# Kernel optimization log

Measured on AMD Instinct MI355X. Metric: run time of the kernel, lower is better.

## Reference

```python
import jax, jax.numpy as jnp
import numpy as np

HID = 512      # LSTM hidden per direction (1024 // 2)
EMB = 768      # BERT hidden size
NUM_TAG = 9
B, S = 64, 512


def setup_inputs() -> dict:
    key = jax.random.key(0)
    ks = jax.random.split(key, 12)
    g = lambda k, sh, sc: (jax.random.normal(k, sh, jnp.float32) * sc)
    return {
        "x": jax.random.normal(ks[0], (B, S, EMB), jnp.float32),
        "mask": jnp.ones((B, S), jnp.int32),
        "target_tag": jax.random.randint(ks[1], (B, S), 0, NUM_TAG, jnp.int32),
        "w_ih_f": g(ks[2], (4 * HID, EMB), 0.02),
        "w_hh_f": g(ks[3], (4 * HID, HID), 0.02),
        "b_f": jnp.zeros((4 * HID,), jnp.float32),
        "w_ih_b": g(ks[4], (4 * HID, EMB), 0.02),
        "w_hh_b": g(ks[5], (4 * HID, HID), 0.02),
        "b_b": jnp.zeros((4 * HID,), jnp.float32),
        "w_out": g(ks[6], (NUM_TAG, 2 * HID), 0.02),
        "b_out": jnp.zeros((NUM_TAG,), jnp.float32),
        "start_trans": g(ks[7], (NUM_TAG,), 0.1),
        "end_trans": g(ks[8], (NUM_TAG,), 0.1),
        "trans": g(ks[9], (NUM_TAG, NUM_TAG), 0.1),
    }


def _lstm_dir(x, w_ih, w_hh, b, reverse):
    # x: [B,S,E] -> outputs [S,B,H]; PyTorch gate order i,f,g,o
    xp = jnp.einsum('bse,ge->sbg', x, w_ih) + b  # precompute input proj [S,B,4H]
    if reverse:
        xp = xp[::-1]
    Bq = x.shape[0]
    def step(carry, xt):
        h, c = carry
        pre = xt + h @ w_hh.T
        i, f, g_, o = jnp.split(pre, 4, axis=-1)
        c = jax.nn.sigmoid(f) * c + jax.nn.sigmoid(i) * jnp.tanh(g_)
        h = jax.nn.sigmoid(o) * jnp.tanh(c)
        return (h, c), h
    init = (jnp.zeros((Bq, HID), x.dtype), jnp.zeros((Bq, HID), x.dtype))
    _, hs = jax.lax.scan(step, init, xp)
    if reverse:
        hs = hs[::-1]
    return hs


def _crf_nll_token_mean(emis, tags, m, start_trans, end_trans, trans):
    # emis: [S,B,T] time-major; tags: [S,B] int; m: [S,B] float (mask)
    Sq, Bq, T = emis.shape
    bidx = jnp.arange(Bq)
    # ---- numerator: score of the gold path ----
    num = start_trans[tags[0]] + emis[0, bidx, tags[0]]
    trans_steps = trans[tags[:-1], tags[1:]]                                   # [S-1,B]
    emit_steps = jnp.take_along_axis(emis[1:], tags[1:, :, None], axis=2)[..., 0]
    num = num + ((trans_steps + emit_steps) * m[1:]).sum(0)
    last_idx = m.sum(0).astype(jnp.int32) - 1                                   # [B]
    num = num + end_trans[tags[last_idx, bidx]]
    # ---- denominator: forward algorithm (log-sum-exp recursion) ----
    alpha0 = start_trans + emis[0]                                              # [B,T]
    def step(alpha, em):
        emis_t, m_t = em
        nxt = jax.nn.logsumexp(alpha[:, :, None] + trans[None] + emis_t[:, None, :], axis=1)
        return jnp.where(m_t[:, None] > 0, nxt, alpha), None
    alpha, _ = jax.lax.scan(step, alpha0, (emis[1:], m[1:]))
    den = jax.nn.logsumexp(alpha + end_trans, axis=1)
    llh = num - den
    return -(llh.sum() / m.sum())  # reduction='token_mean', negated (model loss)


def reference(x, mask, target_tag, w_ih_f, w_hh_f, b_f, w_ih_b, w_hh_b, b_b,
              w_out, b_out, start_trans, end_trans, trans):
    hf = _lstm_dir(x, w_ih_f, w_hh_f, b_f, reverse=False)   # [S,B,H]
    hb = _lstm_dir(x, w_ih_b, w_hh_b, b_b, reverse=True)    # [S,B,H]
    h = jnp.concatenate([hf, hb], axis=-1)                  # [S,B,2H]
    emis = jnp.einsum('sbh,th->sbt', h, w_out) + b_out      # [S,B,T] (dropout=identity in eval)
    tags = target_tag.T                                     # [S,B]
    m = mask.T.astype(emis.dtype)                           # [S,B]
    return _crf_nll_token_mean(emis, tags, m, start_trans, end_trans, trans)
```

## Files before the change

### kernel.cpp

```cpp
#include <hip/hip_runtime.h>
#include <cstdint>
#include <cstddef>

#define SS   512
#define BB   64
#define EMBD 768
#define HIDN 512
#define G4   2048
#define NTAG 9

typedef __attribute__((ext_vector_type(8))) __bf16 bf16x8;
typedef __attribute__((ext_vector_type(4))) float  f32x4;
typedef unsigned long long u64;

union HCast { f32x4 f; bf16x8 h; };

__device__ inline void load_h16_bypass(const void* base, f32x4* f) {
  asm volatile(
    "global_load_dwordx4 %0, %16, off sc0 sc1\n\t"
    "global_load_dwordx4 %1, %16, off offset:64 sc0 sc1\n\t"
    "global_load_dwordx4 %2, %16, off offset:128 sc0 sc1\n\t"
    "global_load_dwordx4 %3, %16, off offset:192 sc0 sc1\n\t"
    "global_load_dwordx4 %4, %16, off offset:256 sc0 sc1\n\t"
    "global_load_dwordx4 %5, %16, off offset:320 sc0 sc1\n\t"
    "global_load_dwordx4 %6, %16, off offset:384 sc0 sc1\n\t"
    "global_load_dwordx4 %7, %16, off offset:448 sc0 sc1\n\t"
    "global_load_dwordx4 %8, %16, off offset:512 sc0 sc1\n\t"
    "global_load_dwordx4 %9, %16, off offset:576 sc0 sc1\n\t"
    "global_load_dwordx4 %10, %16, off offset:640 sc0 sc1\n\t"
    "global_load_dwordx4 %11, %16, off offset:704 sc0 sc1\n\t"
    "global_load_dwordx4 %12, %16, off offset:768 sc0 sc1\n\t"
    "global_load_dwordx4 %13, %16, off offset:832 sc0 sc1\n\t"
    "global_load_dwordx4 %14, %16, off offset:896 sc0 sc1\n\t"
    "global_load_dwordx4 %15, %16, off offset:960 sc0 sc1\n\t"
    "s_waitcnt vmcnt(0)"
    : "=&v"(f[0]), "=&v"(f[1]), "=&v"(f[2]), "=&v"(f[3]),
      "=&v"(f[4]), "=&v"(f[5]), "=&v"(f[6]), "=&v"(f[7]),
      "=&v"(f[8]), "=&v"(f[9]), "=&v"(f[10]), "=&v"(f[11]),
      "=&v"(f[12]), "=&v"(f[13]), "=&v"(f[14]), "=&v"(f[15])
    : "v"(base)
    : "memory");
}
__device__ inline void store_h8_bypass(void* p, u64 v) {
  asm volatile("global_store_dwordx2 %0, %1, off sc0 sc1" :: "v"(p), "v"(v) : "memory");
}
__device__ inline void store_i32_bypass(int* p, int v) {
  asm volatile("global_store_dword %0, %1, off sc0 sc1" :: "v"(p), "v"(v) : "memory");
}
__device__ inline int load_i32_bypass(const int* p) {
  int v;
  asm volatile("global_load_dword %0, %1, off sc0 sc1\n\ts_waitcnt vmcnt(0)"
               : "=v"(v) : "v"(p) : "memory");
  return v;
}

__global__ __launch_bounds__(256) void cvt_kernel(
    const float* __restrict__ src, __bf16* __restrict__ dst, int n8)
{
  int i = blockIdx.x * 256 + threadIdx.x;
  if (i >= n8) return;
  f32x4 a = *reinterpret_cast<const f32x4*>(src + 8 * (size_t)i);
  f32x4 b = *reinterpret_cast<const f32x4*>(src + 8 * (size_t)i + 4);
  bf16x8 o;
  o[0]=(__bf16)a[0]; o[1]=(__bf16)a[1]; o[2]=(__bf16)a[2]; o[3]=(__bf16)a[3];
  o[4]=(__bf16)b[0]; o[5]=(__bf16)b[1]; o[6]=(__bf16)b[2]; o[7]=(__bf16)b[3];
  *reinterpret_cast<bf16x8*>(dst + 8 * (size_t)i) = o;
}

__global__ __launch_bounds__(256, 2) void proj_kernel(
    const __bf16* __restrict__ xb, const __bf16* __restrict__ wfb,
    const __bf16* __restrict__ wbb, const float* __restrict__ bias_f,
    const float* __restrict__ bias_b, float* __restrict__ xp,
    int t0, int chunk)
{
  const int nb = blockIdx.x;
  const int tt = blockIdx.y;
  const int d  = blockIdx.z;
  const int s  = d ? (SS - 1 - (t0 + tt)) : (t0 + tt);
  const __bf16* __restrict__ wih = d ? wbb : wfb;
  const float*  __restrict__ bias = d ? bias_b : bias_f;

  const int t = threadIdx.x, wv = t >> 6, l = t & 63;
  const int quad = l >> 4, col = l & 15;

  const __bf16* brow[8];
  float bj[8];
  const int pbase = 128 * nb;
#pragma unroll
  for (int j = 0; j < 8; j++) {
    int p    = pbase + 16 * j + col;
    int gate = p & 3;
    int hc   = 16 * (p >> 6) + 4 * ((p >> 2) & 3) + ((p >> 4) & 3);
    int g    = gate * HIDN + hc;
    brow[j]  = wih + (size_t)g * EMBD + 8 * quad;
    bj[j]    = bias[g];
  }
  const __bf16* arow = xb + ((size_t)(16 * wv + col) * SS + s) * EMBD + 8 * quad;

  f32x4 acc[8];
#pragma unroll
  for (int j = 0; j < 8; j++) acc[j] = f32x4{0.f, 0.f, 0.f, 0.f};

  for (int kk = 0; kk < 24; kk++) {
    bf16x8 a = *reinterpret_cast<const bf16x8*>(arow + 32 * kk);
#pragma unroll
    for (int j = 0; j < 8; j++) {
      bf16x8 b = *reinterpret_cast<const bf16x8*>(brow[j] + 32 * kk);
      acc[j] = __builtin_amdgcn_mfma_f32_16x16x32_bf16(a, b, acc[j], 0, 0, 0);
    }
  }
  float* xpd = xp + (size_t)(d * chunk + tt) * (size_t)G4 * BB + 16 * wv + 4 * quad;
#pragma unroll
  for (int j = 0; j < 8; j++) {
    int p = pbase + 16 * j + col;
    f32x4 v = acc[j];
    v[0] += bj[j]; v[1] += bj[j]; v[2] += bj[j]; v[3] += bj[j];
    *reinterpret_cast<f32x4*>(xpd + (size_t)p * BB) = v;
  }
}

struct RecCtl {
  int prog[2][64];
  int pad[128];
};

struct RecParams {
  const float* xp;
  const float* whh_f;
  const float* whh_b;
  __bf16* hh;
  float*  cT;
  RecCtl* ctl;
  int     chunk;
};

__global__ __launch_bounds__(256, 1) void rec_kernel(RecParams p)
{
  const int wg   = blockIdx.x;
  const int d    = wg >> 5;
  const int sl   = wg & 31;
  const int t    = threadIdx.x;
  const int wv   = t >> 6;
  const int l    = t & 63;
  const int quad = l >> 4;
  const int col  = l & 15;
  const int hcl  = col >> 2;
  const int gate = col & 3;
  const int j4   = col & 3;

  const float* __restrict__ whh = d ? p.whh_b : p.whh_f;

  bf16x8 bfrag[4][16];
#pragma unroll
  for (int j = 0; j < 4; j++) {
    const int hcb = 16 * sl + 4 * hcl + j;
    const float* wr = whh + (size_t)(gate * HIDN + hcb) * HIDN + 8 * quad;
#pragma unroll
    for (int kk = 0; kk < 16; kk++) {
      f32x4 w0 = *reinterpret_cast<const f32x4*>(wr + 32 * kk);
      f32x4 w1 = *reinterpret_cast<const f32x4*>(wr + 32 * kk + 4);
      bf16x8 v;
      v[0] = (__bf16)w0[0]; v[1] = (__bf16)w0[1]; v[2] = (__bf16)w0[2]; v[3] = (__bf16)w0[3];
      v[4] = (__bf16)w1[0]; v[5] = (__bf16)w1[1]; v[6] = (__bf16)w1[2]; v[7] = (__bf16)w1[3];
      bfrag[j][kk] = v;
    }
  }

  const int bA = 16 * wv + col;
  const int bC = 16 * wv + 4 * quad + gate;
  const int hcs = 16 * sl + 4 * hcl;
  const size_t slotsz = (size_t)BB * HIDN;
  __bf16* hhd = p.hh + (size_t)d * (p.chunk + 1) * slotsz;
  const float* xpd = p.xp + (size_t)d * p.chunk * ((size_t)G4 * BB);

  float c[4];
#pragma unroll
  for (int j = 0; j < 4; j++)
    c[j] = p.cT[((size_t)d * HIDN + hcs + j) * BB + bC];

  f32x4 xpn[4];
#pragma unroll
  for (int j = 0; j < 4; j++)
    xpn[j] = *reinterpret_cast<const f32x4*>(
        xpd + (size_t)(64 * sl + 16 * j + col) * BB + 16 * wv + 4 * quad);

  int* prog = &p.ctl->prog[d][0];
  const int* myslot = prog + (l & 31);

  u64 hword = 0;
  for (int tt = 0; tt < p.chunk; tt++) {
    const char* hbase = (const char*)hhd + (size_t)tt * slotsz * 2
                      + (size_t)bA * (HIDN * 2) + quad * 16;
    f32x4 araw[16];
    load_h16_bypass(hbase, araw);
    bf16x8 afrag[16];
#pragma unroll
    for (int kk = 0; kk < 16; kk++) { HCast hc_; hc_.f = araw[kk]; afrag[kk] = hc_.h; }

    f32x4 acc[4][2];
#pragma unroll
    for (int j = 0; j < 4; j++) {
      acc[j][0] = xpn[j];
      acc[j][1] = f32x4{0.f, 0.f, 0.f, 0.f};
    }
#pragma unroll
    for (int kk = 0; kk < 16; kk += 2) {
#pragma unroll
      for (int j = 0; j < 4; j++) {
        acc[j][0] = __builtin_amdgcn_mfma_f32_16x16x32_bf16(afrag[kk],     bfrag[j][kk],     acc[j][0], 0, 0, 0);
        acc[j][1] = __builtin_amdgcn_mfma_f32_16x16x32_bf16(afrag[kk + 1], bfrag[j][kk + 1], acc[j][1], 0, 0, 0);
      }
    }

    hword = 0;
#pragma unroll
    for (int j = 0; j < 4; j++) {
      float v0 = acc[j][0][0] + acc[j][1][0];
      float v1 = acc[j][0][1] + acc[j][1][1];
      float v2 = acc[j][0][2] + acc[j][1][2];
      float v3 = acc[j][0][3] + acc[j][1][3];
      {
        float t0 = __shfl_xor(v1, 1); float t1 = __shfl_xor(v0, 1);
        float t2 = __shfl_xor(v3, 1); float t3 = __shfl_xor(v2, 1);
        if (j4 & 1) { v0 = t0; v2 = t2; } else { v1 = t1; v3 = t3; }
        float u0 = __shfl_xor(v2, 2); float u1 = __shfl_xor(v3, 2);
        float u2 = __shfl_xor(v0, 2); float u3 = __shfl_xor(v1, 2);
        if (j4 & 2) { v0 = u0; v1 = u1; } else { v2 = u2; v3 = u3; }
      }
      float ig = 1.f / (1.f + __expf(-v0));
      float fg = 1.f / (1.f + __expf(-v1));
      float gg = 1.f - 2.f / (__expf(2.f * v2) + 1.f);
      float og = 1.f / (1.f + __expf(-v3));
      c[j] = fg * c[j] + ig * gg;
      float hn = og * (1.f - 2.f / (__expf(2.f * c[j]) + 1.f));
      union { __bf16 b; unsigned short u; } cv; cv.b = (__bf16)hn;
      hword |= (u64)cv.u << (16 * j);
    }
    store_h8_bypass((char*)hhd + (size_t)(tt + 1) * slotsz * 2
                    + (size_t)bC * (HIDN * 2) + (size_t)hcs * 2, hword);

    if (tt + 1 < p.chunk) {
#pragma unroll
      for (int j = 0; j < 4; j++)
        xpn[j] = *reinterpret_cast<const f32x4*>(
            xpd + (size_t)(tt + 1) * ((size_t)G4 * BB)
            + (size_t)(64 * sl + 16 * j + col) * BB + 16 * wv + 4 * quad);
    }

    __builtin_amdgcn_s_waitcnt(0);
    __syncthreads();
    if (t == 0) store_i32_bypass(prog + sl, tt + 1);
    if (wv == 0) {
      const int tgt = tt + 1;
      while (true) {
        int v = load_i32_bypass(myslot);
        if (__ballot(v >= tgt) == ~0ull) break;
        __builtin_amdgcn_s_sleep(1);
      }
    }
    __syncthreads();
    __atomic_signal_fence(__ATOMIC_SEQ_CST);
  }

  store_h8_bypass((char*)hhd + (size_t)bC * (HIDN * 2) + (size_t)hcs * 2, hword);
#pragma unroll
  for (int j = 0; j < 4; j++)
    p.cT[((size_t)d * HIDN + hcs + j) * BB + bC] = c[j];
}

__global__ __launch_bounds__(256) void emis_kernel(
    const __bf16* __restrict__ hh, const float* __restrict__ w_out,
    float* __restrict__ emis_f, float* __restrict__ emis_b,
    int t0, int chunk)
{
  const int tt = blockIdx.x;
  const int d  = blockIdx.y;
  const int t  = threadIdx.x;
  const int b  = t & 63;
  const int grp = t >> 6;

  const __bf16* hp = hh + ((size_t)d * (chunk + 1) + tt + 1) * ((size_t)BB * HIDN)
                   + (size_t)b * HIDN;
  const float* w0 = w_out + (size_t)grp * (2 * HIDN) + d * HIDN;
  const float* w1 = w_out + (size_t)(grp + 4) * (2 * HIDN) + d * HIDN;
  const float* w2 = w_out + (size_t)8 * (2 * HIDN) + d * HIDN;

  float a0 = 0.f, a1 = 0.f, a2 = 0.f;
  for (int k = 0; k < HIDN; k += 8) {
    bf16x8 hv8 = *reinterpret_cast<const bf16x8*>(hp + k);
#pragma unroll
    for (int j = 0; j < 8; j++) {
      float hv = (float)hv8[j];
      a0 += hv * w0[k + j];
      a1 += hv * w1[k + j];
      a2 += hv * w2[k + j];
    }
  }
  const int sidx = (d == 0) ? (t0 + tt) : (SS - 1 - (t0 + tt));
  float* dst = d ? emis_b : emis_f;
  dst[((size_t)sidx * BB + b) * NTAG + grp]     = a0;
  dst[((size_t)sidx * BB + b) * NTAG + grp + 4] = a1;
  if (grp == 0) dst[((size_t)sidx * BB + b) * NTAG + 8] = a2;
}

__global__ __launch_bounds__(64) void crf_kernel(
    const float* __restrict__ emis_f, const float* __restrict__ emis_b,
    const float* __restrict__ b_out, const float* __restrict__ start_tr,
    const float* __restrict__ end_tr, const float* __restrict__ trans,
    const int* __restrict__ mask, const int* __restrict__ target,
    float* __restrict__ llh)
{
  const int b    = blockIdx.x;
  const int lane = threadIdx.x;

  auto E = [&](int s, int tg) -> float {
    size_t o = ((size_t)s * BB + b) * NTAG + tg;
    return emis_f[o] + emis_b[o] + b_out[tg];
  };

  float numpart = 0.f;
  int msum = 0;
  for (int s = lane; s < SS; s += 64) {
    int m = mask[b * SS + s];
    msum += m;
    if (s >= 1 && m > 0) {
      int tp = target[b * SS + s - 1];
      int tc = target[b * SS + s];
      numpart += trans[tp * NTAG + tc] + E(s, tc);
    }
  }
#pragma unroll
  for (int off = 32; off > 0; off >>= 1) {
    numpart += __shfl_down(numpart, off, 64);
    msum    += __shfl_down(msum, off, 64);
  }

  const int tc = lane;
  const bool act = (tc < NTAG);
  float trc[NTAG] = {0.f};
  float alpha = 0.f;
  if (act) {
#pragma unroll
    for (int i = 0; i < NTAG; i++) trc[i] = trans[i * NTAG + tc];
    alpha = start_tr[tc] + E(0, tc);
  }
  for (int s = 1; s < SS; s++) {
    float e = act ? E(s, tc) : 0.f;
    float av[NTAG];
    float mx = -3.0e30f;
#pragma unroll
    for (int i = 0; i < NTAG; i++) {
      av[i] = __shfl(alpha, i, 64) + trc[i];
      mx = fmaxf(mx, av[i]);
    }
    float sum = 0.f;
#pragma unroll
    for (int i = 0; i < NTAG; i++) sum += __expf(av[i] - mx);
    float nxt = mx + __logf(sum) + e;
    if (act && mask[b * SS + s] > 0) alpha = nxt;
  }
  float fv = act ? (alpha + end_tr[tc]) : -3.0e30f;
  float q[NTAG];
  float mx2 = -3.0e30f;
#pragma unroll
  for (int i = 0; i < NTAG; i++) {
    q[i] = __shfl(fv, i, 64);
    mx2 = fmaxf(mx2, q[i]);
  }
  float s2 = 0.f;
#pragma unroll
  for (int i = 0; i < NTAG; i++) s2 += __expf(q[i] - mx2);
  float den = mx2 + __logf(s2);

  if (lane == 0) {
    int last = msum - 1;
    int tg0 = target[b * SS + 0];
    int tgl = target[b * SS + last];
    float num = start_tr[tg0] + E(0, tg0) + numpart + end_tr[tgl];
    llh[b] = num - den;
  }
}

__global__ __launch_bounds__(256) void fin_kernel(
    const float* __restrict__ llh, const int* __restrict__ mask,
    float* __restrict__ out)
{
  __shared__ float sf[256];
  __shared__ int   si[256];
  const int t = threadIdx.x;
  float a = (t < BB) ? llh[t] : 0.f;
  int m = 0;
  for (int i = t; i < BB * SS; i += 256) m += mask[i];
  sf[t] = a; si[t] = m;
  __syncthreads();
  for (int o = 128; o > 0; o >>= 1) {
    if (t < o) { sf[t] += sf[t + o]; si[t] += si[t + o]; }
    __syncthreads();
  }
  if (t == 0) out[0] = -(sf[0] / (float)si[0]);
}

extern "C" void kernel_launch(void* const* d_in, const int* in_sizes, int n_in,
                              void* d_out, int out_size, void* d_ws, size_t ws_size,
                              hipStream_t stream)
{
  const float* x     = (const float*)d_in[0];
  const int*   mask  = (const int*)d_in[1];
  const int*   targ  = (const int*)d_in[2];
  const float* wih_f = (const float*)d_in[3];
  const float* whh_f = (const float*)d_in[4];
  const float* b_f   = (const float*)d_in[5];
  const float* wih_b = (const float*)d_in[6];
  const float* whh_b = (const float*)d_in[7];
  const float* b_b   = (const float*)d_in[8];
  const float* w_out = (const float*)d_in[9];
  const float* b_out = (const float*)d_in[10];
  const float* st    = (const float*)d_in[11];
  const float* et    = (const float*)d_in[12];
  const float* tr    = (const float*)d_in[13];
  float* out = (float*)d_out;

  const size_t nxb   = (size_t)BB * SS * EMBD;
  const size_t nwb   = (size_t)G4 * EMBD;
  const size_t ctl_i = sizeof(RecCtl) / 4;
  const size_t fixed_f = (size_t)2 * SS * BB * NTAG + 64 + (size_t)2 * HIDN * BB
                       + ctl_i + nxb / 2 + nwb;
  int chunk = 1;
  for (int c = SS; c >= 1; c >>= 1) {
    size_t need = fixed_f * 4 + (size_t)c * 2 * G4 * BB * 4
                + (size_t)2 * (c + 1) * BB * HIDN * 2;
    if (need <= ws_size) { chunk = c; break; }
  }

  float* fp = (float*)d_ws;
  float* emis_f = fp; fp += (size_t)SS * BB * NTAG;
  float* emis_b = fp; fp += (size_t)SS * BB * NTAG;
  float* llh    = fp; fp += 64;
  float* cT     = fp; fp += (size_t)2 * HIDN * BB;
  RecCtl* ctl   = (RecCtl*)fp; fp += ctl_i;
  __bf16* xb16  = (__bf16*)fp; fp += nxb / 2;
  __bf16* wfb16 = (__bf16*)fp; fp += nwb / 2;
  __bf16* wbb16 = (__bf16*)fp; fp += nwb / 2;
  float* xp     = fp; fp += (size_t)chunk * 2 * G4 * BB;
  __bf16* hh    = (__bf16*)fp;

  {
    int n8 = (int)(nxb / 8);
    cvt_kernel<<<dim3((n8 + 255) / 256), 256, 0, stream>>>(x, xb16, n8);
    int w8 = (int)(nwb / 8);
    cvt_kernel<<<dim3((w8 + 255) / 256), 256, 0, stream>>>(wih_f, wfb16, w8);
    cvt_kernel<<<dim3((w8 + 255) / 256), 256, 0, stream>>>(wih_b, wbb16, w8);
  }

  const size_t slotsz = (size_t)BB * HIDN;
  hipMemsetAsync(cT, 0, (size_t)2 * HIDN * BB * sizeof(float), stream);
  hipMemsetAsync(hh, 0, slotsz * sizeof(__bf16), stream);
  hipMemsetAsync(hh + (size_t)(chunk + 1) * slotsz, 0, slotsz * sizeof(__bf16), stream);

  const int nch = SS / chunk;
  for (int c = 0; c < nch; c++) {
    const int t0 = c * chunk;
    hipMemsetAsync(ctl, 0, sizeof(RecCtl), stream);
    proj_kernel<<<dim3(16, chunk, 2), 256, 0, stream>>>(
        xb16, wfb16, wbb16, b_f, b_b, xp, t0, chunk);
    RecParams rp{xp, whh_f, whh_b, hh, cT, ctl, chunk};
    void* ka[] = {&rp};
    hipLaunchCooperativeKernel(rec_kernel, dim3(64), dim3(256), ka, 0, stream);
    emis_kernel<<<dim3(chunk, 2), 256, 0, stream>>>(
        hh, w_out, emis_f, emis_b, t0, chunk);
  }
  crf_kernel<<<dim3(64), 64, 0, stream>>>(emis_f, emis_b, b_out, st, et, tr, mask, targ, llh);
  fin_kernel<<<dim3(1), 256, 0, stream>>>(llh, mask, out);
}
```

Baseline: 5.007 ms.

## Replace per-step progress-counter barrier with data-flag polling on hidden-state buffer

Before the recurrence, each workgroup fills the hidden-state history slots with an all-ones sentinel and runs a single one-time barrier. The per-timestep grid-wide progress-counter barrier is removed. Instead each wave reloads its h slice until no word equals the sentinel, so synchronisation becomes point-to-point through the data itself. This removes a global barrier round-trip per step, at the cost of an extra fill pass over the buffer and a reliance on bypass-cache visibility and on no real bf16 pair ever matching the sentinel pattern.

New measurement: 5.216 ms. 4.2% more time.

```diff
diff --git a/kernel.cpp b/kernel.cpp
--- a/kernel.cpp
+++ b/kernel.cpp
@@ -14,6 +14,7 @@
 typedef unsigned long long u64;
 
 union HCast { f32x4 f; bf16x8 h; };
+union UCast { f32x4 f; unsigned u[4]; };
 
 __device__ inline void load_h16_bypass(const void* base, f32x4* f) {
   asm volatile(
@@ -148,6 +149,32 @@
   const int gate = col & 3;
   const int j4   = col & 3;
 
+  const size_t slotsz = (size_t)BB * HIDN;
+
+  {
+    const size_t qper = (size_t)p.chunk * slotsz / 4;
+    const size_t totq = 2 * qper;
+    const size_t gtid = (size_t)wg * 256 + t;
+    for (size_t q = gtid; q < totq; q += (size_t)64 * 256) {
+      const size_t dd  = q / qper;
+      const size_t off = q - dd * qper;
+      char* dst = (char*)p.hh + (dd * (p.chunk + 1) + 1) * slotsz * 2 + off * 8;
+      store_h8_bypass(dst, 0xFFFFFFFFFFFFFFFFull);
+    }
+    __builtin_amdgcn_s_waitcnt(0);
+    __syncthreads();
+    if (t == 0) store_i32_bypass(&p.ctl->prog[0][wg], 1);
+    if (wv == 0) {
+      const int* slot = &p.ctl->prog[0][l];
+      while (true) {
+        int v = load_i32_bypass(slot);
+        if (__ballot(v != 0) == ~0ull) break;
+        __builtin_amdgcn_s_sleep(1);
+      }
+    }
+    __syncthreads();
+  }
+
   const float* __restrict__ whh = d ? p.whh_b : p.whh_f;
 
   bf16x8 bfrag[4][16];
@@ -169,7 +196,6 @@
   const int bA = 16 * wv + col;
   const int bC = 16 * wv + 4 * quad + gate;
   const int hcs = 16 * sl + 4 * hcl;
-  const size_t slotsz = (size_t)BB * HIDN;
   __bf16* hhd = p.hh + (size_t)d * (p.chunk + 1) * slotsz;
   const float* xpd = p.xp + (size_t)d * p.chunk * ((size_t)G4 * BB);
 
@@ -183,16 +209,26 @@
   for (int j = 0; j < 4; j++)
     xpn[j] = *reinterpret_cast<const f32x4*>(
         xpd + (size_t)(64 * sl + 16 * j + col) * BB + 16 * wv + 4 * quad);
-
-  int* prog = &p.ctl->prog[d][0];
-  const int* myslot = prog + (l & 31);
 
   u64 hword = 0;
   for (int tt = 0; tt < p.chunk; tt++) {
     const char* hbase = (const char*)hhd + (size_t)tt * slotsz * 2
                       + (size_t)bA * (HIDN * 2) + quad * 16;
     f32x4 araw[16];
-    load_h16_bypass(hbase, araw);
+    for (;;) {
+      load_h16_bypass(hbase, araw);
+      unsigned mx = 0u;
+#pragma unroll
+      for (int kk = 0; kk < 16; kk++) {
+        UCast q; q.f = araw[kk];
+        unsigned a01 = q.u[0] > q.u[1] ? q.u[0] : q.u[1];
+        unsigned a23 = q.u[2] > q.u[3] ? q.u[2] : q.u[3];
+        unsigned am  = a01 > a23 ? a01 : a23;
+        mx = mx > am ? mx : am;
+      }
+      if (__all(mx != 0xFFFFFFFFu)) break;
+      __builtin_amdgcn_s_sleep(1);
+    }
     bf16x8 afrag[16];
 #pragma unroll
     for (int kk = 0; kk < 16; kk++) { HCast hc_; hc_.f = araw[kk]; afrag[kk] = hc_.h; }
@@ -246,26 +282,28 @@
             xpd + (size_t)(tt + 1) * ((size_t)G4 * BB)
             + (size_t)(64 * sl + 16 * j + col) * BB + 16 * wv + 4 * quad);
     }
-
+  }
+
+  if (p.chunk == 1) {
     __builtin_amdgcn_s_waitcnt(0);
     __syncthreads();
-    if (t == 0) store_i32_bypass(prog + sl, tt + 1);
+    if (t == 0) store_i32_bypass(&p.ctl->prog[1][wg], 1);
     if (wv == 0) {
-      const int tgt = tt + 1;
+      const int* slot = &p.ctl->prog[1][l];
       while (true) {
-        int v = load_i32_bypass(myslot);
-        if (__ballot(v >= tgt) == ~0ull) break;
+        int v = load_i32_bypass(slot);
+        if (__ballot(v != 0) == ~0ull) break;
         __builtin_amdgcn_s_sleep(1);
       }
     }
     __syncthreads();
-    __atomic_signal_fence(__ATOMIC_SEQ_CST);
   }
 
   store_h8_bypass((char*)hhd + (size_t)bC * (HIDN * 2) + (size_t)hcs * 2, hword);
 #pragma unroll
   for (int j = 0; j < 4; j++)
     p.cT[((size_t)d * HIDN + hcs + j) * BB + bC] = c[j];
+  __builtin_amdgcn_s_waitcnt(0);
 }
 
 __global__ __launch_bounds__(256) void emis_kernel(
```
